# Performance work log

Hardware: AMD Instinct MI355X
Metric: run time of the kernel (lower is better)

## Reference

```python
import jax, jax.numpy as jnp
import numpy as np

B, N = 16384, 32
OBS0, OBS1, OBS2 = 16, 64, 16
D = 64          # hidden dim / single_head_dim
H = 3           # n_heads
NACT = 2


def setup_inputs() -> dict:
    key = jax.random.key(0)
    ks = jax.random.split(key, 32)
    w = lambda i, shape: jax.random.normal(ks[i], shape, jnp.float32) * 0.05
    return {
        "s0": jax.random.normal(ks[0], (B, OBS0), jnp.float32),
        "s1": jax.random.normal(ks[1], (B, OBS1), jnp.float32),
        "s2": jax.random.normal(ks[2], (B, N, OBS2), jnp.float32),
        "W_own": w(3, (D, OBS0)), "b_own": w(4, (D,)),
        "W_env": w(5, (D, OBS1)), "b_env": w(6, (D,)),
        "W_s1": w(7, (D, OBS2)), "b_s1": w(8, (D,)),
        "W_s2": w(9, (D, D)),    "b_s2": w(10, (D,)),
        "W_q": w(11, (D, D)), "W_k": w(12, (D, D)), "W_v": w(13, (D, D)),
        "W_cq": w(14, (D, D)), "W_ck": w(15, (D, D)), "W_cv": w(16, (D, D)),
        "W_mo": w(17, (128, H * D)), "b_mo": w(18, (128,)),
        "W_a1": w(19, (64, 128)), "b_a1": w(20, (64,)),
        "W_a2": w(21, (NACT, 64)), "b_a2": w(22, (NACT,)),
    }


def reference(s0, s1, s2, W_own, b_own, W_env, b_env, W_s1, b_s1, W_s2, b_s2,
              W_q, W_k, W_v, W_cq, W_ck, W_cv, W_mo, b_mo, W_a1, b_a1, W_a2, b_a2):
    # branch encoders
    own_e = jax.nn.relu(s0 @ W_own.T + b_own)            # [B, 64]
    env_e = jax.nn.relu(s1 @ W_env.T + b_env)            # [B, 64]
    h = jax.nn.relu(s2 @ W_s1.T + b_s1)                  # [B, N, 64]
    intru_e = jax.nn.relu(h @ W_s2.T + b_s2)             # [B, N, 64]

    # masked single-head attention pooling over neighbors
    q = own_e @ W_q.T                                    # [B, 64]
    k = intru_e @ W_k.T                                  # [B, N, 64]
    v = intru_e @ W_v.T                                  # [B, N, 64]
    mask = jnp.mean(intru_e, axis=2, keepdims=True) != 0  # [B, N, 1] (bool of mean)
    score = jnp.einsum('bnd,bd->bn', k, q)[..., None]    # [B, N, 1]
    score = jnp.where(mask, score, -jnp.inf)
    alpha = jax.nn.softmax(score / np.sqrt(D).astype(np.float32), axis=1)
    alpha = jnp.where(mask, alpha, 0.0)
    v_att = jnp.sum(v * alpha, axis=1)                   # [B, 64]

    concat = jnp.concatenate([own_e, env_e, v_att], axis=1)  # [B, 192]

    # degenerate multi-head self-attention over seq_len=1
    b = concat.shape[0]
    raw = concat.reshape(b, 1, H, D)                     # [B, 1, H, D]
    comQ = (raw @ W_cq.T).transpose(0, 2, 1, 3)          # [B, H, 1, D]
    comK = (raw @ W_ck.T).transpose(0, 2, 1, 3)
    comV = (raw @ W_cv.T).transpose(0, 2, 1, 3)
    product = jnp.einsum('bhsd,bhtd->bhst', comQ, comK) / np.sqrt(D).astype(np.float32)
    attn = jax.nn.softmax(product, axis=-1)              # [B, H, 1, 1] == 1
    scores = attn @ comV                                 # [B, H, 1, D]
    concat_m = scores.transpose(0, 2, 1, 3).reshape(b, 1, H * D)  # [B, 1, 192]

    mo = concat_m @ W_mo.T + b_mo                        # [B, 1, 128]
    a = jax.nn.relu(mo @ W_a1.T + b_a1)                  # [B, 1, 64]
    return jnp.tanh(a @ W_a2.T + b_a2)                   # [B, 1, n_actions]
```

## Files before the change

### kernel.cpp

```cpp
#include <hip/hip_runtime.h>
#include <hip/hip_bf16.h>
#include <math.h>


typedef __attribute__((ext_vector_type(8))) short short8;
typedef __attribute__((ext_vector_type(4))) float f32x4;

#define WS_A1F   0
#define WS_A2F   1024
#define WS_AOWN  3072
#define WS_AENV  4096
#define WS_AQK   6144
#define WS_FOLDF 8192
#define WS_A1FR  20480
#define WS_SETUP_END 24576
#define WS_WCVV  24576

static __device__ inline unsigned pk2(float a, float b) {
    union { __hip_bfloat162 h; unsigned u; } cv;
    cv.h = __float22bfloat162_rn(make_float2(a, b));
    return cv.u;
}

static __device__ inline float rowquad_sum(float x) {
    float a = x, b = x;
    asm("v_permlane16_swap_b32 %0, %1" : "+v"(a), "+v"(b));
    float y = a + b;
    float c = y, d = y;
    asm("v_permlane32_swap_b32 %0, %1" : "+v"(c), "+v"(d));
    return c + d;
}

__global__ void actor_wcvv(const float* __restrict__ wCv,
                           const float* __restrict__ wV,
                           float* __restrict__ ws)
{
    int t = blockIdx.x * 256 + threadIdx.x;
    int out = t >> 3, sl = t & 7;
    int c = out >> 6, d = out & 63;
    float acc = 0.f;
    #pragma unroll
    for (int i = 0; i < 8; ++i) {
        int e = sl * 8 + i;
        acc = fmaf(wCv[c * 64 + e], wV[e * 64 + d], acc);
    }
    acc += __shfl_xor(acc, 1, 64);
    acc += __shfl_xor(acc, 2, 64);
    acc += __shfl_xor(acc, 4, 64);
    if (sl == 0) ws[WS_WCVV + out] = acc;
}

__global__ void actor_setup_pack(
    const float* __restrict__ wOwn, const float* __restrict__ wEnv,
    const float* __restrict__ wS1,  const float* __restrict__ wS2,
    const float* __restrict__ wA1,  float* __restrict__ ws)
{
    int t = blockIdx.x * 256 + threadIdx.x;
    unsigned* wsu = reinterpret_cast<unsigned*>(ws);
    if (t < 1024) {
        int ht = t >> 8, rem = t & 255, lane = rem >> 2, jj = rem & 3;
        int qq = lane >> 4, m = lane & 15;
        int row = ht * 16 + m, k0 = qq * 8 + jj * 2;
        float v0 = (k0 < 16) ? wS1[row * 16 + k0]     : 0.f;
        float v1 = (k0 < 16) ? wS1[row * 16 + k0 + 1] : 0.f;
        wsu[WS_A1F + t] = pk2(v0, v1);
    } else if (t < 3072) {
        int u = t - 1024;
        int f = u >> 8, rem = u & 255, lane = rem >> 2, jj = rem & 3;
        int qq = lane >> 4, m = lane & 15;
        int dt = f >> 1, kt = f & 1;
        int row = dt * 16 + m, k = kt * 32 + qq * 8 + jj * 2;
        wsu[WS_A2F + u] = pk2(wS2[row * 64 + k], wS2[row * 64 + k + 1]);
    } else if (t < 4096) {
        int u = t - 3072;
        int ht = u >> 8, rem = u & 255, lane = rem >> 2, jj = rem & 3;
        int qq = lane >> 4, m = lane & 15;
        int row = ht * 16 + m, k0 = qq * 8 + jj * 2;
        float v0 = (k0 < 16) ? wOwn[row * 16 + k0]     : 0.f;
        float v1 = (k0 < 16) ? wOwn[row * 16 + k0 + 1] : 0.f;
        wsu[WS_AOWN + u] = pk2(v0, v1);
    } else if (t < 6144) {
        int u = t - 4096;
        int f = u >> 8, rem = u & 255, lane = rem >> 2, jj = rem & 3;
        int qq = lane >> 4, m = lane & 15;
        int ht = f >> 1, kt = f & 1;
        int row = ht * 16 + m, k = kt * 32 + qq * 8 + jj * 2;
        wsu[WS_AENV + u] = pk2(wEnv[row * 64 + k], wEnv[row * 64 + k + 1]);
    } else {
        int u = t - 6144;
        int f = u >> 8, rem = u & 255, lane = rem >> 2, jj = rem & 3;
        int rt = f >> 2, kt = f & 3;
        int row = rt * 16 + (lane & 15);
        int k = kt * 32 + (lane >> 4) * 8 + jj * 2;
        wsu[WS_A1FR + u] = pk2(wA1[row * 128 + k], wA1[row * 128 + k + 1]);
    }
}

__global__ void actor_setup_gemm(
    const float* __restrict__ wQ,  const float* __restrict__ wK,
    const float* __restrict__ wCv, const float* __restrict__ wMo,
    float* __restrict__ ws)
{
    int t = blockIdx.x * 256 + threadIdx.x;
    unsigned* wsu = reinterpret_cast<unsigned*>(ws);
    if (t < 98304) {
        int u = t >> 3, sl = t & 7;
        int f = u >> 8, rem = u & 255, lane = rem >> 2, jj = rem & 3;
        int RT = f / 6, kt = f - RT * 6;
        int row = RT * 16 + (lane & 15);
        int k = kt * 32 + (lane >> 4) * 8 + jj * 2;
        int h = k >> 6, dp = k & 63;
        const float* wmr = wMo + row * 192 + h * 64;
        const float* rhs = (h == 2) ? (ws + WS_WCVV) : wCv;
        float a0 = 0.f, a1 = 0.f;
        #pragma unroll
        for (int i = 0; i < 8; ++i) {
            int d = sl * 8 + i;
            float m = wmr[d];
            a0 = fmaf(m, rhs[d * 64 + dp],     a0);
            a1 = fmaf(m, rhs[d * 64 + dp + 1], a1);
        }
        a0 += __shfl_xor(a0, 1, 64); a0 += __shfl_xor(a0, 2, 64); a0 += __shfl_xor(a0, 4, 64);
        a1 += __shfl_xor(a1, 1, 64); a1 += __shfl_xor(a1, 2, 64); a1 += __shfl_xor(a1, 4, 64);
        if (sl == 0) wsu[WS_FOLDF + u] = pk2(a0, a1);
    } else {
        int v = t - 98304;
        int u = v >> 3, sl = v & 7;
        int f = u >> 8, rem = u & 255, lane = rem >> 2, jj = rem & 3;
        int qq = lane >> 4, m = lane & 15;
        int dt = f >> 1, kt = f & 1;
        int dp = dt * 16 + m;
        int e = kt * 32 + qq * 8 + jj * 2;
        float a0 = 0.f, a1 = 0.f;
        #pragma unroll
        for (int i = 0; i < 8; ++i) {
            int d = sl * 8 + i;
            float kd = wK[d * 64 + dp];
            a0 = fmaf(wQ[d * 64 + e],     kd, a0);
            a1 = fmaf(wQ[d * 64 + e + 1], kd, a1);
        }
        a0 += __shfl_xor(a0, 1, 64); a0 += __shfl_xor(a0, 2, 64); a0 += __shfl_xor(a0, 4, 64);
        a1 += __shfl_xor(a1, 1, 64); a1 += __shfl_xor(a1, 2, 64); a1 += __shfl_xor(a1, 4, 64);
        if (sl == 0) wsu[WS_AQK + u] = pk2(a0, a1);
    }
}

__global__ __launch_bounds__(256, 3) void actor_mega(
    const float* __restrict__ s0g, const float* __restrict__ s1g,
    const float* __restrict__ s2g,
    const float* __restrict__ bOwn, const float* __restrict__ bEnv,
    const float* __restrict__ bS1g, const float* __restrict__ bS2g,
    const float* __restrict__ bMo,  const float* __restrict__ bA1,
    const float* __restrict__ wA2,  const float* __restrict__ bA2,
    const float* __restrict__ ws,   float* __restrict__ outg)
{
    __shared__ char   xbL[16 * 384];
    __shared__ float  qkL[16][72];
    __shared__ ushort Hl[4][2][16 * 72];
    __shared__ ushort TR[16 * 72];
    __shared__ char   mbL[16 * 256];
    __shared__ float  aL[16][66];

    const int tid  = threadIdx.x;
    const int wid  = tid >> 6;
    const int lane = tid & 63;
    const int q    = lane >> 4;
    const int r    = lane & 15;
    const int swzr = (r & 7) << 4;
    const int eb   = blockIdx.x * 16;
    const f32x4 z = {0.f, 0.f, 0.f, 0.f};

    {
        short8 Ao = reinterpret_cast<const short8*>(ws + WS_AOWN)[wid * 64 + lane];
        const float* sp = s0g + (size_t)(eb + r) * 16 + (q & 1) * 8;
        float4 sa = *reinterpret_cast<const float4*>(sp);
        float4 sb = *reinterpret_cast<const float4*>(sp + 4);
        union { short8 s8; unsigned u[4]; } B;
        B.u[0] = pk2(sa.x, sa.y); B.u[1] = pk2(sa.z, sa.w);
        B.u[2] = pk2(sb.x, sb.y); B.u[3] = pk2(sb.z, sb.w);
        f32x4 c = *reinterpret_cast<const f32x4*>(bOwn + wid * 16 + q * 4);
        f32x4 D = __builtin_amdgcn_mfma_f32_16x16x32_bf16(Ao, B.s8, c, 0, 0, 0);
        unsigned p0 = pk2(fmaxf(D[0], 0.f), fmaxf(D[1], 0.f));
        unsigned p1 = pk2(fmaxf(D[2], 0.f), fmaxf(D[3], 0.f));
        *reinterpret_cast<uint2*>(xbL + r * 384 + ((wid * 32 + q * 8) ^ swzr)) =
            make_uint2(p0, p1);
        *reinterpret_cast<uint2*>(reinterpret_cast<char*>(TR) + r * 144 + wid * 32 + q * 8) =
            make_uint2(p0, p1);
    }
    {
        short8 Ae0 = reinterpret_cast<const short8*>(ws + WS_AENV)[(wid * 2 + 0) * 64 + lane];
        short8 Ae1 = reinterpret_cast<const short8*>(ws + WS_AENV)[(wid * 2 + 1) * 64 + lane];
        const float* sb1 = s1g + (size_t)(eb + r) * 64;
        f32x4 D = *reinterpret_cast<const f32x4*>(bEnv + wid * 16 + q * 4);
        {
            float4 sa = *reinterpret_cast<const float4*>(sb1 + q * 8);
            float4 sb = *reinterpret_cast<const float4*>(sb1 + q * 8 + 4);
            union { short8 s8; unsigned u[4]; } B;
            B.u[0] = pk2(sa.x, sa.y); B.u[1] = pk2(sa.z, sa.w);
            B.u[2] = pk2(sb.x, sb.y); B.u[3] = pk2(sb.z, sb.w);
            D = __builtin_amdgcn_mfma_f32_16x16x32_bf16(Ae0, B.s8, D, 0, 0, 0);
        }
        {
            float4 sa = *reinterpret_cast<const float4*>(sb1 + 32 + q * 8);
            float4 sb = *reinterpret_cast<const float4*>(sb1 + 32 + q * 8 + 4);
            union { short8 s8; unsigned u[4]; } B;
            B.u[0] = pk2(sa.x, sa.y); B.u[1] = pk2(sa.z, sa.w);
            B.u[2] = pk2(sb.x, sb.y); B.u[3] = pk2(sb.z, sb.w);
            D = __builtin_amdgcn_mfma_f32_16x16x32_bf16(Ae1, B.s8, D, 0, 0, 0);
        }
        unsigned p0 = pk2(fmaxf(D[0], 0.f), fmaxf(D[1], 0.f));
        unsigned p1 = pk2(fmaxf(D[2], 0.f), fmaxf(D[3], 0.f));
        *reinterpret_cast<uint2*>(xbL + r * 384 + ((128 + wid * 32 + q * 8) ^ swzr)) =
            make_uint2(p0, p1);
    }
    __syncthreads();

    {
        short8 Aq0 = reinterpret_cast<const short8*>(ws + WS_AQK)[(wid * 2 + 0) * 64 + lane];
        short8 Aq1 = reinterpret_cast<const short8*>(ws + WS_AQK)[(wid * 2 + 1) * 64 + lane];
        const char* trb = reinterpret_cast<const char*>(TR) + r * 144;
        short8 B0 = *reinterpret_cast<const short8*>(trb + q * 16);
        short8 B1 = *reinterpret_cast<const short8*>(trb + 64 + q * 16);
        f32x4 D = __builtin_amdgcn_mfma_f32_16x16x32_bf16(Aq0, B0, z, 0, 0, 0);
        D = __builtin_amdgcn_mfma_f32_16x16x32_bf16(Aq1, B1, D, 0, 0, 0);
        *reinterpret_cast<f32x4*>(&qkL[r][wid * 16 + q * 4]) = D;
    }
    __syncthreads();

    short8 A1[4], A2[8];
    {
        const short8* p1 = reinterpret_cast<const short8*>(ws + WS_A1F);
        #pragma unroll
        for (int ht = 0; ht < 4; ++ht) A1[ht] = p1[ht * 64 + lane];
        const short8* p2 = reinterpret_cast<const short8*>(ws + WS_A2F);
        #pragma unroll
        for (int f = 0; f < 8; ++f) A2[f] = p2[f * 64 + lane];
    }
    f32x4 b1c[4], b2c[4];
    #pragma unroll
    for (int t4 = 0; t4 < 4; ++t4) {
        b1c[t4] = *reinterpret_cast<const f32x4*>(bS1g + t4 * 16 + q * 4);
        b2c[t4] = *reinterpret_cast<const f32x4*>(bS2g + t4 * 16 + q * 4);
    }
    const int el   = r >> 2;
    const int j    = r & 3;
    const int sloc = wid * 4 + el;

    float qkf[16];
    #pragma unroll
    for (int dt = 0; dt < 4; ++dt) {
        f32x4 v = *reinterpret_cast<const f32x4*>(&qkL[sloc][dt * 16 + q * 4]);
        qkf[dt*4+0] = v[0]; qkf[dt*4+1] = v[1]; qkf[dt*4+2] = v[2]; qkf[dt*4+3] = v[3];
    }
    const float* s2base = s2g + (size_t)(eb + sloc) * 512 + (q & 1) * 8;

    float den = 0.f;
    f32x4 Pac[4] = {{0,0,0,0},{0,0,0,0},{0,0,0,0},{0,0,0,0}};

    #pragma unroll 2
    for (int it = 0; it < 8; ++it) {
        const float* sp = s2base + (it * 4 + j) * 16;
        float4 sa = *reinterpret_cast<const float4*>(sp);
        float4 sb = *reinterpret_cast<const float4*>(sp + 4);
        union { short8 s8; unsigned u[4]; } B1;
        B1.u[0] = pk2(sa.x, sa.y); B1.u[1] = pk2(sa.z, sa.w);
        B1.u[2] = pk2(sb.x, sb.y); B1.u[3] = pk2(sb.z, sb.w);

        f32x4 hD[4];
        #pragma unroll
        for (int ht = 0; ht < 4; ++ht)
            hD[ht] = __builtin_amdgcn_mfma_f32_16x16x32_bf16(A1[ht], B1.s8, b1c[ht], 0, 0, 0);

        ushort* hrow = &Hl[wid][it & 1][r * 72];
        #pragma unroll
        for (int ht = 0; ht < 4; ++ht) {
            float h0 = fmaxf(hD[ht][0], 0.f), h1 = fmaxf(hD[ht][1], 0.f);
            float h2 = fmaxf(hD[ht][2], 0.f), h3 = fmaxf(hD[ht][3], 0.f);
            *reinterpret_cast<uint2*>(hrow + ht * 16 + q * 4) =
                make_uint2(pk2(h0, h1), pk2(h2, h3));
        }
        short8 B2a = *reinterpret_cast<const short8*>(hrow + q * 8);
        short8 B2b = *reinterpret_cast<const short8*>(hrow + 32 + q * 8);

        f32x4 iD[4];
        #pragma unroll
        for (int dt = 0; dt < 4; ++dt) {
            f32x4 c0 = __builtin_amdgcn_mfma_f32_16x16x32_bf16(A2[dt*2+0], B2a, b2c[dt], 0, 0, 0);
            iD[dt]   = __builtin_amdgcn_mfma_f32_16x16x32_bf16(A2[dt*2+1], B2b, c0, 0, 0, 0);
        }
        float rs = 0.f, sc = 0.f;
        #pragma unroll
        for (int dt = 0; dt < 4; ++dt) {
            #pragma unroll
            for (int i = 0; i < 4; ++i) {
                float x = fmaxf(iD[dt][i], 0.f);
                iD[dt][i] = x;
                rs += x;
                sc = fmaf(x, qkf[dt*4+i], sc);
            }
        }
        sc = rowquad_sum(sc);
        rs = rowquad_sum(rs);
        float w = (rs != 0.f) ? __expf(sc * 0.125f) : 0.f;
        den += w;
        #pragma unroll
        for (int dt = 0; dt < 4; ++dt)
            #pragma unroll
            for (int i = 0; i < 4; ++i)
                Pac[dt][i] = fmaf(w, iD[dt][i], Pac[dt][i]);
    }
    #pragma unroll
    for (int m = 1; m <= 2; m <<= 1) {
        den += __shfl_xor(den, m, 64);
        #pragma unroll
        for (int dt = 0; dt < 4; ++dt)
            #pragma unroll
            for (int i = 0; i < 4; ++i)
                Pac[dt][i] += __shfl_xor(Pac[dt][i], m, 64);
    }
    {
        float inv = (den > 0.f) ? (1.f / den) : 0.f;
        if (j == 0) {
            const int swzs = (sloc & 7) << 4;
            #pragma unroll
            for (int dt = 0; dt < 4; ++dt) {
                float p0 = Pac[dt][0] * inv, p1 = Pac[dt][1] * inv;
                float p2 = Pac[dt][2] * inv, p3 = Pac[dt][3] * inv;
                *reinterpret_cast<uint2*>(xbL + sloc * 384 + ((256 + dt * 32 + q * 8) ^ swzs)) =
                    make_uint2(pk2(p0, p1), pk2(p2, p3));
            }
        }
    }
    __syncthreads();

    {
        const short8* fp = reinterpret_cast<const short8*>(ws + WS_FOLDF);
        short8 Amo0[6], Amo1[6];
        #pragma unroll
        for (int kt = 0; kt < 6; ++kt) {
            Amo0[kt] = fp[((wid * 2 + 0) * 6 + kt) * 64 + lane];
            Amo1[kt] = fp[((wid * 2 + 1) * 6 + kt) * 64 + lane];
        }
        short8 Bf[6];
        #pragma unroll
        for (int kt = 0; kt < 6; ++kt)
            Bf[kt] = *reinterpret_cast<const short8*>(
                xbL + r * 384 + ((kt * 64 + q * 16) ^ swzr));
        f32x4 D0 = z, D1 = z;
        #pragma unroll
        for (int kt = 0; kt < 6; ++kt) {
            D0 = __builtin_amdgcn_mfma_f32_16x16x32_bf16(Amo0[kt], Bf[kt], D0, 0, 0, 0);
            D1 = __builtin_amdgcn_mfma_f32_16x16x32_bf16(Amo1[kt], Bf[kt], D1, 0, 0, 0);
        }
        f32x4 bm0 = *reinterpret_cast<const f32x4*>(bMo + wid * 32 + q * 4);
        f32x4 bm1 = *reinterpret_cast<const f32x4*>(bMo + wid * 32 + 16 + q * 4);
        char* wp0 = mbL + r * 256 + ((wid * 64 + q * 8) ^ swzr);
        *reinterpret_cast<unsigned*>(wp0)     = pk2(D0[0] + bm0[0], D0[1] + bm0[1]);
        *reinterpret_cast<unsigned*>(wp0 + 4) = pk2(D0[2] + bm0[2], D0[3] + bm0[3]);
        char* wp1 = mbL + r * 256 + ((wid * 64 + 32 + q * 8) ^ swzr);
        *reinterpret_cast<unsigned*>(wp1)     = pk2(D1[0] + bm1[0], D1[1] + bm1[1]);
        *reinterpret_cast<unsigned*>(wp1 + 4) = pk2(D1[2] + bm1[2], D1[3] + bm1[3]);
    }
    __syncthreads();

    {
        const short8* ap = reinterpret_cast<const short8*>(ws + WS_A1FR);
        f32x4 D = z;
        #pragma unroll
        for (int kt = 0; kt < 4; ++kt) {
            short8 Ak = ap[(wid * 4 + kt) * 64 + lane];
            short8 Bk = *reinterpret_cast<const short8*>(
                mbL + r * 256 + ((kt * 64 + q * 16) ^ swzr));
            D = __builtin_amdgcn_mfma_f32_16x16x32_bf16(Ak, Bk, D, 0, 0, 0);
        }
        f32x4 ba = *reinterpret_cast<const f32x4*>(bA1 + wid * 16 + q * 4);
        float a0 = fmaxf(D[0] + ba[0], 0.f), a1v = fmaxf(D[1] + ba[1], 0.f);
        float a2v = fmaxf(D[2] + ba[2], 0.f), a3v = fmaxf(D[3] + ba[3], 0.f);
        *reinterpret_cast<float2*>(&aL[r][wid * 16 + q * 4])     = make_float2(a0, a1v);
        *reinterpret_cast<float2*>(&aL[r][wid * 16 + q * 4 + 2]) = make_float2(a2v, a3v);
    }
    __syncthreads();

    if (tid < 32) {
        const int s = tid & 15, o = tid >> 4;
        const float* wr = wA2 + o * 64;
        float p = 0.f;
        #pragma unroll
        for (int d = 0; d < 64; ++d) p = fmaf(aL[s][d], wr[d], p);
        outg[(size_t)(eb + s) * 2 + o] = tanhf(p + bA2[o]);
    }
}

extern "C" void kernel_launch(void* const* d_in, const int* in_sizes, int n_in,
                              void* d_out, int out_size, void* d_ws, size_t ws_size,
                              hipStream_t stream) {
    const float* s0   = (const float*)d_in[0];
    const float* s1   = (const float*)d_in[1];
    const float* s2   = (const float*)d_in[2];
    const float* wOwn = (const float*)d_in[3];
    const float* bOwn = (const float*)d_in[4];
    const float* wEnv = (const float*)d_in[5];
    const float* bEnv = (const float*)d_in[6];
    const float* wS1  = (const float*)d_in[7];
    const float* bS1  = (const float*)d_in[8];
    const float* wS2  = (const float*)d_in[9];
    const float* bS2  = (const float*)d_in[10];
    const float* wQ   = (const float*)d_in[11];
    const float* wK   = (const float*)d_in[12];
    const float* wV   = (const float*)d_in[13];
    const float* wCv  = (const float*)d_in[16];
    const float* wMo  = (const float*)d_in[17];
    const float* bMo  = (const float*)d_in[18];
    const float* wA1  = (const float*)d_in[19];
    const float* bA1  = (const float*)d_in[20];
    const float* wA2  = (const float*)d_in[21];
    const float* bA2  = (const float*)d_in[22];
    float* ws  = (float*)d_ws;
    float* out = (float*)d_out;

    hipLaunchKernelGGL(actor_wcvv, dim3(128), dim3(256), 0, stream, wCv, wV, ws);
    hipLaunchKernelGGL(actor_setup_pack, dim3(40), dim3(256), 0, stream,
                       wOwn, wEnv, wS1, wS2, wA1, ws);
    hipLaunchKernelGGL(actor_setup_gemm, dim3(448), dim3(256), 0, stream,
                       wQ, wK, wCv, wMo, ws);
    hipLaunchKernelGGL(actor_mega, dim3(16384 / 16), dim3(256), 0, stream,
                       s0, s1, s2, bOwn, bEnv, bS1, bS2, bMo, bA1, wA2, bA2,
                       ws, out);
}
```

Baseline: 40.25 us.

## Merge setup kernels and compute prologue redundantly per wave to drop barriers

Merges the Wcv·Wv product kernel and the weight-pack kernel into one launch, removing one kernel launch. In the main kernel each wave now computes all four output tiles of the own, env and qk prologue GEMMs, using a private transpose buffer per wave and writing shared results only for its own rows. This removes two block-wide __syncthreads but does four times the prologue MFMA work and weight loads. The Hl double buffer also shrinks to a single buffer per wave, which cuts LDS use but relies on wave-local ordering for reuse.

Result: slower. 42.71 us (+6.1%).

```diff
diff --git a/kernel.cpp b/kernel.cpp
--- a/kernel.cpp
+++ b/kernel.cpp
@@ -31,32 +31,30 @@
     return c + d;
 }
 
-__global__ void actor_wcvv(const float* __restrict__ wCv,
-                           const float* __restrict__ wV,
-                           float* __restrict__ ws)
-{
-    int t = blockIdx.x * 256 + threadIdx.x;
-    int out = t >> 3, sl = t & 7;
-    int c = out >> 6, d = out & 63;
-    float acc = 0.f;
-    #pragma unroll
-    for (int i = 0; i < 8; ++i) {
-        int e = sl * 8 + i;
-        acc = fmaf(wCv[c * 64 + e], wV[e * 64 + d], acc);
-    }
-    acc += __shfl_xor(acc, 1, 64);
-    acc += __shfl_xor(acc, 2, 64);
-    acc += __shfl_xor(acc, 4, 64);
-    if (sl == 0) ws[WS_WCVV + out] = acc;
-}
-
-__global__ void actor_setup_pack(
+__global__ void actor_prep1(
+    const float* __restrict__ wCv,  const float* __restrict__ wV,
     const float* __restrict__ wOwn, const float* __restrict__ wEnv,
     const float* __restrict__ wS1,  const float* __restrict__ wS2,
     const float* __restrict__ wA1,  float* __restrict__ ws)
 {
-    int t = blockIdx.x * 256 + threadIdx.x;
     unsigned* wsu = reinterpret_cast<unsigned*>(ws);
+    if (blockIdx.x < 128) {
+        int t = blockIdx.x * 256 + threadIdx.x;
+        int out = t >> 3, sl = t & 7;
+        int c = out >> 6, d = out & 63;
+        float acc = 0.f;
+        #pragma unroll
+        for (int i = 0; i < 8; ++i) {
+            int e = sl * 8 + i;
+            acc = fmaf(wCv[c * 64 + e], wV[e * 64 + d], acc);
+        }
+        acc += __shfl_xor(acc, 1, 64);
+        acc += __shfl_xor(acc, 2, 64);
+        acc += __shfl_xor(acc, 4, 64);
+        if (sl == 0) ws[WS_WCVV + out] = acc;
+        return;
+    }
+    int t = (blockIdx.x - 128) * 256 + threadIdx.x;
     if (t < 1024) {
         int ht = t >> 8, rem = t & 255, lane = rem >> 2, jj = rem & 3;
         int qq = lane >> 4, m = lane & 15;
@@ -156,8 +154,8 @@
 {
     __shared__ char   xbL[16 * 384];
     __shared__ float  qkL[16][72];
-    __shared__ ushort Hl[4][2][16 * 72];
-    __shared__ ushort TR[16 * 72];
+    __shared__ ushort Hl[4][16 * 72];
+    __shared__ ushort TR[4][16 * 72];
     __shared__ char   mbL[16 * 256];
     __shared__ float  aL[16][66];
 
@@ -168,64 +166,73 @@
     const int r    = lane & 15;
     const int swzr = (r & 7) << 4;
     const int eb   = blockIdx.x * 16;
+    const bool own_row = ((r >> 2) == wid);
     const f32x4 z = {0.f, 0.f, 0.f, 0.f};
 
     {
-        short8 Ao = reinterpret_cast<const short8*>(ws + WS_AOWN)[wid * 64 + lane];
         const float* sp = s0g + (size_t)(eb + r) * 16 + (q & 1) * 8;
         float4 sa = *reinterpret_cast<const float4*>(sp);
         float4 sb = *reinterpret_cast<const float4*>(sp + 4);
         union { short8 s8; unsigned u[4]; } B;
         B.u[0] = pk2(sa.x, sa.y); B.u[1] = pk2(sa.z, sa.w);
         B.u[2] = pk2(sb.x, sb.y); B.u[3] = pk2(sb.z, sb.w);
-        f32x4 c = *reinterpret_cast<const f32x4*>(bOwn + wid * 16 + q * 4);
-        f32x4 D = __builtin_amdgcn_mfma_f32_16x16x32_bf16(Ao, B.s8, c, 0, 0, 0);
-        unsigned p0 = pk2(fmaxf(D[0], 0.f), fmaxf(D[1], 0.f));
-        unsigned p1 = pk2(fmaxf(D[2], 0.f), fmaxf(D[3], 0.f));
-        *reinterpret_cast<uint2*>(xbL + r * 384 + ((wid * 32 + q * 8) ^ swzr)) =
-            make_uint2(p0, p1);
-        *reinterpret_cast<uint2*>(reinterpret_cast<char*>(TR) + r * 144 + wid * 32 + q * 8) =
-            make_uint2(p0, p1);
-    }
-    {
-        short8 Ae0 = reinterpret_cast<const short8*>(ws + WS_AENV)[(wid * 2 + 0) * 64 + lane];
-        short8 Ae1 = reinterpret_cast<const short8*>(ws + WS_AENV)[(wid * 2 + 1) * 64 + lane];
+        char* trw = reinterpret_cast<char*>(TR[wid]) + r * 144;
+        const short8* Aop = reinterpret_cast<const short8*>(ws + WS_AOWN);
+        #pragma unroll
+        for (int ht = 0; ht < 4; ++ht) {
+            short8 Ao = Aop[ht * 64 + lane];
+            f32x4 c = *reinterpret_cast<const f32x4*>(bOwn + ht * 16 + q * 4);
+            f32x4 D = __builtin_amdgcn_mfma_f32_16x16x32_bf16(Ao, B.s8, c, 0, 0, 0);
+            unsigned p0 = pk2(fmaxf(D[0], 0.f), fmaxf(D[1], 0.f));
+            unsigned p1 = pk2(fmaxf(D[2], 0.f), fmaxf(D[3], 0.f));
+            *reinterpret_cast<uint2*>(trw + ht * 32 + q * 8) = make_uint2(p0, p1);
+            if (own_row)
+                *reinterpret_cast<uint2*>(xbL + r * 384 + ((ht * 32 + q * 8) ^ swzr)) =
+                    make_uint2(p0, p1);
+        }
+    }
+    {
         const float* sb1 = s1g + (size_t)(eb + r) * 64;
-        f32x4 D = *reinterpret_cast<const f32x4*>(bEnv + wid * 16 + q * 4);
+        union { short8 s8; unsigned u[4]; } B0, B1;
         {
             float4 sa = *reinterpret_cast<const float4*>(sb1 + q * 8);
             float4 sb = *reinterpret_cast<const float4*>(sb1 + q * 8 + 4);
-            union { short8 s8; unsigned u[4]; } B;
-            B.u[0] = pk2(sa.x, sa.y); B.u[1] = pk2(sa.z, sa.w);
-            B.u[2] = pk2(sb.x, sb.y); B.u[3] = pk2(sb.z, sb.w);
-            D = __builtin_amdgcn_mfma_f32_16x16x32_bf16(Ae0, B.s8, D, 0, 0, 0);
+            B0.u[0] = pk2(sa.x, sa.y); B0.u[1] = pk2(sa.z, sa.w);
+            B0.u[2] = pk2(sb.x, sb.y); B0.u[3] = pk2(sb.z, sb.w);
         }
         {
             float4 sa = *reinterpret_cast<const float4*>(sb1 + 32 + q * 8);
             float4 sb = *reinterpret_cast<const float4*>(sb1 + 32 + q * 8 + 4);
-            union { short8 s8; unsigned u[4]; } B;
-            B.u[0] = pk2(sa.x, sa.y); B.u[1] = pk2(sa.z, sa.w);
-            B.u[2] = pk2(sb.x, sb.y); B.u[3] = pk2(sb.z, sb.w);
-            D = __builtin_amdgcn_mfma_f32_16x16x32_bf16(Ae1, B.s8, D, 0, 0, 0);
-        }
-        unsigned p0 = pk2(fmaxf(D[0], 0.f), fmaxf(D[1], 0.f));
-        unsigned p1 = pk2(fmaxf(D[2], 0.f), fmaxf(D[3], 0.f));
-        *reinterpret_cast<uint2*>(xbL + r * 384 + ((128 + wid * 32 + q * 8) ^ swzr)) =
-            make_uint2(p0, p1);
-    }
-    __syncthreads();
-
-    {
-        short8 Aq0 = reinterpret_cast<const short8*>(ws + WS_AQK)[(wid * 2 + 0) * 64 + lane];
-        short8 Aq1 = reinterpret_cast<const short8*>(ws + WS_AQK)[(wid * 2 + 1) * 64 + lane];
-        const char* trb = reinterpret_cast<const char*>(TR) + r * 144;
+            B1.u[0] = pk2(sa.x, sa.y); B1.u[1] = pk2(sa.z, sa.w);
+            B1.u[2] = pk2(sb.x, sb.y); B1.u[3] = pk2(sb.z, sb.w);
+        }
+        const short8* Aep = reinterpret_cast<const short8*>(ws + WS_AENV);
+        #pragma unroll
+        for (int ht = 0; ht < 4; ++ht) {
+            f32x4 D = *reinterpret_cast<const f32x4*>(bEnv + ht * 16 + q * 4);
+            D = __builtin_amdgcn_mfma_f32_16x16x32_bf16(Aep[(ht*2+0)*64 + lane], B0.s8, D, 0, 0, 0);
+            D = __builtin_amdgcn_mfma_f32_16x16x32_bf16(Aep[(ht*2+1)*64 + lane], B1.s8, D, 0, 0, 0);
+            if (own_row) {
+                unsigned p0 = pk2(fmaxf(D[0], 0.f), fmaxf(D[1], 0.f));
+                unsigned p1 = pk2(fmaxf(D[2], 0.f), fmaxf(D[3], 0.f));
+                *reinterpret_cast<uint2*>(xbL + r * 384 + ((128 + ht * 32 + q * 8) ^ swzr)) =
+                    make_uint2(p0, p1);
+            }
+        }
+    }
+    {
+        const char* trb = reinterpret_cast<const char*>(TR[wid]) + r * 144;
         short8 B0 = *reinterpret_cast<const short8*>(trb + q * 16);
         short8 B1 = *reinterpret_cast<const short8*>(trb + 64 + q * 16);
-        f32x4 D = __builtin_amdgcn_mfma_f32_16x16x32_bf16(Aq0, B0, z, 0, 0, 0);
-        D = __builtin_amdgcn_mfma_f32_16x16x32_bf16(Aq1, B1, D, 0, 0, 0);
-        *reinterpret_cast<f32x4*>(&qkL[r][wid * 16 + q * 4]) = D;
-    }
-    __syncthreads();
+        const short8* Aqp = reinterpret_cast<const short8*>(ws + WS_AQK);
+        #pragma unroll
+        for (int dt = 0; dt < 4; ++dt) {
+            f32x4 D = __builtin_amdgcn_mfma_f32_16x16x32_bf16(Aqp[(dt*2+0)*64 + lane], B0, z, 0, 0, 0);
+            D = __builtin_amdgcn_mfma_f32_16x16x32_bf16(Aqp[(dt*2+1)*64 + lane], B1, D, 0, 0, 0);
+            if (own_row)
+                *reinterpret_cast<f32x4*>(&qkL[r][dt * 16 + q * 4]) = D;
+        }
+    }
 
     short8 A1[4], A2[8];
     {
@@ -271,7 +278,7 @@
         for (int ht = 0; ht < 4; ++ht)
             hD[ht] = __builtin_amdgcn_mfma_f32_16x16x32_bf16(A1[ht], B1.s8, b1c[ht], 0, 0, 0);
 
-        ushort* hrow = &Hl[wid][it & 1][r * 72];
+        ushort* hrow = &Hl[wid][r * 72];
         #pragma unroll
         for (int ht = 0; ht < 4; ++ht) {
             float h0 = fmaxf(hD[ht][0], 0.f), h1 = fmaxf(hD[ht][1], 0.f);
@@ -418,9 +425,8 @@
     float* ws  = (float*)d_ws;
     float* out = (float*)d_out;
 
-    hipLaunchKernelGGL(actor_wcvv, dim3(128), dim3(256), 0, stream, wCv, wV, ws);
-    hipLaunchKernelGGL(actor_setup_pack, dim3(40), dim3(256), 0, stream,
-                       wOwn, wEnv, wS1, wS2, wA1, ws);
+    hipLaunchKernelGGL(actor_prep1, dim3(168), dim3(256), 0, stream,
+                       wCv, wV, wOwn, wEnv, wS1, wS2, wA1, ws);
     hipLaunchKernelGGL(actor_setup_gemm, dim3(448), dim3(256), 0, stream,
                        wQ, wK, wCv, wMo, ws);
     hipLaunchKernelGGL(actor_mega, dim3(16384 / 16), dim3(256), 0, stream,
```
